# Optimization experiments

Hardware: AMD Instinct MI355X
Metric: run time of the kernel (lower is better)

## Reference

```python
import jax, jax.numpy as jnp
import numpy as np

ALPHA = 0.2  # LeakyReLU negative slope

B, K, F = 64, 100, 128   # batch, window_size (=num_nodes), n_features
E = 2 * K                 # embed_dim*2 = 200 (embed_dim defaults to window_size)


def setup_inputs() -> dict:
    key = jax.random.key(0)
    k1, k2, k3, k4, k5 = jax.random.split(key, 5)
    x = jax.random.normal(k1, (B, K, F), dtype=jnp.float32)
    # lin: Linear(2F -> E); store weight as (2F, E) so projection is x @ W
    W = jax.random.normal(k2, (2 * F, E), dtype=jnp.float32) * (1.0 / np.sqrt(2 * F))
    b = jax.random.normal(k3, (E,), dtype=jnp.float32) * 0.01
    # attention vector a: (E, 1) in torch; use (E,)
    a = jax.random.normal(k4, (E,), dtype=jnp.float32) * (1.414 / np.sqrt(E))
    bias = jax.random.normal(k5, (K, K), dtype=jnp.float32) * 0.01
    return {"x": x, "W": W, "b": b, "a": a, "bias": bias}


def reference(x, W, b, a, bias):
    F_ = x.shape[-1]
    # lin(concat(left, right)) == left @ W[:F] + right @ W[F:] + b;
    # compute the two projections once each instead of materializing the
    # (B, K, K, 2F) pairwise concat tensor.
    left_p = jnp.einsum('bkf,fe->bke', x, W[:F_])    # (B, K, E)
    right_p = jnp.einsum('bkf,fe->bke', x, W[F_:])   # (B, K, E)
    pre = left_p[:, :, None, :] + right_p[:, None, :, :] + b  # (B, K, K, E)
    act = jnp.where(pre > 0, pre, ALPHA * pre)                # LeakyReLU
    e = jnp.einsum('bije,e->bij', act, a) + bias              # (B, K, K)
    attention = jax.nn.softmax(e, axis=2)
    h = jax.nn.sigmoid(jnp.einsum('bij,bjf->bif', attention, x))  # (B, K, F)
    return h
```

## Files before the change

kernel.cpp:

```cpp
#include <hip/hip_runtime.h>

typedef _Float16 half_t;
typedef _Float16 h2 __attribute__((ext_vector_type(2)));
typedef unsigned int uint32;

#define K_ 100
#define F_ 128
#define E_ 200

#if defined(__has_builtin)
#if __has_builtin(__builtin_amdgcn_fdot2)
#define FDOT2(a,b,c) __builtin_amdgcn_fdot2((a),(b),(c),false)
#endif
#endif
#ifndef FDOT2
#define FDOT2(a,b,c) fmaf((float)(a).y,(float)(b).y, fmaf((float)(a).x,(float)(b).x,(c)))
#endif

__device__ __forceinline__ h2 bch2(uint32 u){ return __builtin_bit_cast(h2,u); }
__device__ __forceinline__ uint32 pkh2(float a, float b){
  h2 p; p.x=(half_t)a; p.y=(half_t)b; return __builtin_bit_cast(uint32,p);
}

#define LH_OFF 0
#define RH_OFF 640000
#define AH_OFF 1280000
#define AL_OFF 1280128
#define AR_OFF 1286528
#define XJ_OFF 1292928

__global__ __launch_bounds__(256) void k_proj(
    const float* __restrict__ x, const float* __restrict__ W,
    const float* __restrict__ bvec, const float* __restrict__ avec,
    uint32* __restrict__ ws)
{
  const int t  = threadIdx.x;
  const int r0 = (int)blockIdx.x * 10;

  __shared__ __align__(16) uint32 xsh[10 * 64];
  __shared__ float red[20][100];

  for (int u = t; u < 640; u += 256) {
    int row = u >> 6, f2 = u & 63;
    const float* xp = x + (size_t)(r0 + row) * F_ + 2 * f2;
    xsh[row * 64 + f2] = pkh2(xp[0], xp[1]);
  }
  if (blockIdx.x == 0 && t < 100)
    ws[AH_OFF + t] = pkh2(avec[2*t], avec[2*t+1]);
  __syncthreads();

  for (int u = t; u < 640; u += 256) {
    int f = u & 127, lp = u >> 7;
    uint32 u0 = xsh[(2*lp)     * 64 + (f >> 1)];
    uint32 u1 = xsh[(2*lp + 1) * 64 + (f >> 1)];
    int sh = (f & 1) * 16;
    ws[XJ_OFF + (size_t)(r0/2 + lp) * 128 + f] =
        ((u0 >> sh) & 0xffffu) | (((u1 >> sh) & 0xffffu) << 16);
  }

  if (t < 200) {
    const bool isR = (t >= 100);
    const int e2 = isR ? (t - 100) : t;
    const float* Wp = W + (size_t)(isR ? 128 : 0) * E_ + 2 * e2;

    float acc0[10], acc1[10];
    #pragma unroll
    for (int r = 0; r < 10; ++r) { acc0[r] = 0.f; acc1[r] = 0.f; }

    #pragma unroll
    for (int q = 0; q < 16; ++q) {
      uint32 w0u[4], w1u[4];
      #pragma unroll
      for (int fp = 0; fp < 4; ++fp) {
        const float* p0 = Wp + (size_t)(8*q + 2*fp) * E_;
        float2 Av = *(const float2*)p0;
        float2 Bv = *(const float2*)(p0 + E_);
        w0u[fp] = pkh2(Av.x, Bv.x);
        w1u[fp] = pkh2(Av.y, Bv.y);
      }
      #pragma unroll
      for (int r = 0; r < 10; ++r) {
        uint4 xq = *(const uint4*)(xsh + r * 64 + 4 * q);
        acc0[r] = FDOT2(bch2(xq.x), bch2(w0u[0]), acc0[r]);
        acc0[r] = FDOT2(bch2(xq.y), bch2(w0u[1]), acc0[r]);
        acc0[r] = FDOT2(bch2(xq.z), bch2(w0u[2]), acc0[r]);
        acc0[r] = FDOT2(bch2(xq.w), bch2(w0u[3]), acc0[r]);
        acc1[r] = FDOT2(bch2(xq.x), bch2(w1u[0]), acc1[r]);
        acc1[r] = FDOT2(bch2(xq.y), bch2(w1u[1]), acc1[r]);
        acc1[r] = FDOT2(bch2(xq.z), bch2(w1u[2]), acc1[r]);
        acc1[r] = FDOT2(bch2(xq.w), bch2(w1u[3]), acc1[r]);
      }
    }
    if (isR) {
      float b0 = bvec[2 * e2], b1 = bvec[2 * e2 + 1];
      #pragma unroll
      for (int r = 0; r < 10; ++r) { acc0[r] += b0; acc1[r] += b1; }
    }
    h2 a2 = bch2(pkh2(avec[2*e2], avec[2*e2+1]));
    uint32* dst = ws + (isR ? RH_OFF : LH_OFF);
    #pragma unroll
    for (int r = 0; r < 10; ++r) {
      uint32 pr = pkh2(acc0[r], acc1[r]);
      dst[(size_t)(r0 + r) * 100 + e2] = pr;
      red[(isR ? 10 : 0) + r][e2] = FDOT2(a2, bch2(pr), 0.f);
    }
  }
  __syncthreads();

  if (t < 20) {
    float s = 0.f;
    const float* rp = red[t];
    for (int k = 0; k < 100; ++k) s += rp[k];
    float* dstf = (float*)(ws + (t >= 10 ? AR_OFF : AL_OFF));
    dstf[r0 + (t % 10)] = s;
  }
}

#define STEP(lu, au, r0u, r1u, r2u, r3u)                                   \
  do {                                                                     \
    h2 a2 = bch2(au); h2 l2 = bch2(lu); h2 mm;                             \
    mm = __builtin_elementwise_min(l2 + bch2(r0u), z2); acc[0] = FDOT2(a2, mm, acc[0]); \
    mm = __builtin_elementwise_min(l2 + bch2(r1u), z2); acc[1] = FDOT2(a2, mm, acc[1]); \
    mm = __builtin_elementwise_min(l2 + bch2(r2u), z2); acc[2] = FDOT2(a2, mm, acc[2]); \
    mm = __builtin_elementwise_min(l2 + bch2(r3u), z2); acc[3] = FDOT2(a2, mm, acc[3]); \
  } while (0)

#define RPAD 104
#define LPAD 108

__global__ __launch_bounds__(256) void k_main(
    const float* __restrict__ x, const float* __restrict__ bias,
    const uint32* __restrict__ ws, float* __restrict__ out)
{
  const int t  = threadIdx.x;
  const int i0 = (int)blockIdx.x * 10;
  const int b  = (int)blockIdx.y;

  __shared__ __align__(16) uint32 Rsh[100 * RPAD];
  __shared__ __align__(16) uint32 Lsh[10 * LPAD];
  __shared__ uint32 Ash[100];
  __shared__ float  att[10 * 100];
  __shared__ uint32 att2[10 * 50];
  __shared__ float  scratch[256];
  __shared__ float  rowmax[10], rowinv[10];

  const bool act = (t < 250);
  const int ti = act ? (t % 10) : 0;
  const int tj = act ? (t / 10) : 0;

  {
    const uint32* Rb = ws + RH_OFF + (size_t)b * K_ * 100;
    for (int u = t; u < 2500; u += 256) {
      int row = u / 25, c4 = (u % 25) * 4;
      *(uint4*)(&Rsh[row * RPAD + c4]) = *(const uint4*)(Rb + (size_t)row * 100 + c4);
    }
    const uint32* Lb = ws + LH_OFF + (size_t)(b * K_ + i0) * 100;
    if (t < 250) {
      int row = t / 25, c4 = (t % 25) * 4;
      *(uint4*)(&Lsh[row * LPAD + c4]) = *(const uint4*)(Lb + (size_t)row * 100 + c4);
    }
    if (t < 100) Ash[t] = ws[AH_OFF + t];
  }
  __syncthreads();

  float acc[4] = {0.f,0.f,0.f,0.f};
  h2 z2; z2.x = (half_t)0; z2.y = (half_t)0;

  if (act) {
    const uint32* Lp  = Lsh + ti * LPAD;
    const uint32* Rp0 = Rsh + tj * RPAD;
    const uint32* Rp1 = Rsh + (tj + 25) * RPAD;
    const uint32* Rp2 = Rsh + (tj + 50) * RPAD;
    const uint32* Rp3 = Rsh + (tj + 75) * RPAD;
    #pragma unroll 5
    for (int q = 0; q < 25; ++q) {
      uint4 Lq  = *(const uint4*)(Lp  + 4*q);
      uint4 Aq  = *(const uint4*)(Ash + 4*q);
      uint4 R0q = *(const uint4*)(Rp0 + 4*q);
      uint4 R1q = *(const uint4*)(Rp1 + 4*q);
      uint4 R2q = *(const uint4*)(Rp2 + 4*q);
      uint4 R3q = *(const uint4*)(Rp3 + 4*q);
      STEP(Lq.x, Aq.x, R0q.x, R1q.x, R2q.x, R3q.x);
      STEP(Lq.y, Aq.y, R0q.y, R1q.y, R2q.y, R3q.y);
      STEP(Lq.z, Aq.z, R0q.z, R1q.z, R2q.z, R3q.z);
      STEP(Lq.w, Aq.w, R0q.w, R1q.w, R2q.w, R3q.w);
    }
  }

  float v[4];
  if (act) {
    const float* ALf = (const float*)(ws + AL_OFF);
    const float* ARf = (const float*)(ws + AR_OFF);
    float al = ALf[b*K_ + i0 + ti];
    #pragma unroll
    for (int s = 0; s < 4; ++s) {
      int j = tj + 25*s;
      float lv = al + ARf[b*K_ + j] + bias[(i0 + ti)*K_ + j] - 0.8f*acc[s];
      v[s] = fminf(fmaxf(lv, -30000.f), 30000.f);
    }
  }

  {
    float m = -3.0e38f;
    if (act) {
      #pragma unroll
      for (int s = 0; s < 4; ++s) m = fmaxf(m, v[s]);
    }
    scratch[t] = m;
    __syncthreads();
    if (t < 10) {
      float mm = scratch[t];
      for (int k = 1; k < 25; ++k) mm = fmaxf(mm, scratch[t + 10*k]);
      rowmax[t] = mm;
    }
    __syncthreads();
    float ssum = 0.f;
    if (act) {
      float m2 = rowmax[ti];
      #pragma unroll
      for (int s = 0; s < 4; ++s) ssum += __expf(v[s] - m2);
    }
    scratch[t] = ssum;
    __syncthreads();
    if (t < 10) {
      float s2 = 0.f;
      for (int k = 0; k < 25; ++k) s2 += scratch[t + 10*k];
      rowinv[t] = 1.f / s2;
    }
    __syncthreads();
  }
  if (act) {
    float m = rowmax[ti], inv = rowinv[ti];
    #pragma unroll
    for (int s = 0; s < 4; ++s)
      att[ti*K_ + tj + 25*s] = __expf(v[s] - m) * inv;
  }
  __syncthreads();
  for (int u = t; u < 500; u += 256) {
    int i = u / 50, jp = u - i*50;
    att2[i*50 + jp] = pkh2(att[i*K_ + 2*jp], att[i*K_ + 2*jp + 1]);
  }
  __syncthreads();

  {
    const int f = t & 127, ig = t >> 7;
    const uint32* XJ = ws + XJ_OFF + (size_t)(b*50) * 128;
    float z[5];
    #pragma unroll
    for (int m = 0; m < 5; ++m) z[m] = 0.f;
    for (int jp = 0; jp < 50; ++jp) {
      h2 xv = bch2(XJ[jp*128 + f]);
      #pragma unroll
      for (int m = 0; m < 5; ++m) {
        h2 av = bch2(att2[(ig*5 + m)*50 + jp]);
        z[m] = FDOT2(av, xv, z[m]);
      }
    }
    #pragma unroll
    for (int m = 0; m < 5; ++m) {
      int i = ig*5 + m;
      out[(size_t)(b*K_ + i0 + i)*F_ + f] = 1.f / (1.f + __expf(-z[m]));
    }
  }
}

extern "C" void kernel_launch(void* const* d_in, const int* in_sizes, int n_in,
                              void* d_out, int out_size, void* d_ws, size_t ws_size,
                              hipStream_t stream)
{
  const float* x    = (const float*)d_in[0];
  const float* W    = (const float*)d_in[1];
  const float* bvec = (const float*)d_in[2];
  const float* avec = (const float*)d_in[3];
  const float* bias = (const float*)d_in[4];
  float* out  = (float*)d_out;
  uint32* ws  = (uint32*)d_ws;

  k_proj<<<dim3(640),    dim3(256), 0, stream>>>(x, W, bvec, avec, ws);
  k_main<<<dim3(10, 64), dim3(256), 0, stream>>>(x, bias, ws, out);
}
```

Measured before the change: 98.35 us.

## Process two query rows per thread in k_main and parallelize projection reduction

Each k_main block now handles 20 query rows instead of 10, with every thread accumulating scores for two rows. This reuses each loaded R tile from shared memory across two rows and halves the number of times the per-batch R matrix is staged, while halving the grid to 320 blocks. The aggregation stage computes 10 output rows per thread. The 100-element serial sum at the end of k_proj is split into a two-level tree reduction. The cost is more registers and fewer blocks, which may reduce occupancy and load balance across CUs.

```diff
diff --git a/kernel.cpp b/kernel.cpp
--- a/kernel.cpp
+++ b/kernel.cpp
@@ -39,6 +39,7 @@
 
   __shared__ __align__(16) uint32 xsh[10 * 64];
   __shared__ float red[20][100];
+  __shared__ float red2[20 * 10];
 
   for (int u = t; u < 640; u += 256) {
     int row = u >> 6, f2 = u & 63;
@@ -107,22 +108,28 @@
   }
   __syncthreads();
 
+  if (t < 200) {
+    int rr = t / 10, seg = t % 10;
+    const float* rp = red[rr] + seg * 10;
+    float s = 0.f;
+    #pragma unroll
+    for (int k = 0; k < 10; ++k) s += rp[k];
+    red2[rr * 10 + seg] = s;
+  }
+  __syncthreads();
   if (t < 20) {
     float s = 0.f;
-    const float* rp = red[t];
-    for (int k = 0; k < 100; ++k) s += rp[k];
+    #pragma unroll
+    for (int k = 0; k < 10; ++k) s += red2[t * 10 + k];
     float* dstf = (float*)(ws + (t >= 10 ? AR_OFF : AL_OFF));
     dstf[r0 + (t % 10)] = s;
   }
 }
 
-#define STEP(lu, au, r0u, r1u, r2u, r3u)                                   \
+#define STEPA(A_, lu, au, ru)                                              \
   do {                                                                     \
-    h2 a2 = bch2(au); h2 l2 = bch2(lu); h2 mm;                             \
-    mm = __builtin_elementwise_min(l2 + bch2(r0u), z2); acc[0] = FDOT2(a2, mm, acc[0]); \
-    mm = __builtin_elementwise_min(l2 + bch2(r1u), z2); acc[1] = FDOT2(a2, mm, acc[1]); \
-    mm = __builtin_elementwise_min(l2 + bch2(r2u), z2); acc[2] = FDOT2(a2, mm, acc[2]); \
-    mm = __builtin_elementwise_min(l2 + bch2(r3u), z2); acc[3] = FDOT2(a2, mm, acc[3]); \
+    h2 mm = __builtin_elementwise_min(bch2(lu) + bch2(ru), z2);            \
+    A_ = FDOT2(bch2(au), mm, A_);                                          \
   } while (0)
 
 #define RPAD 104
@@ -133,19 +140,19 @@
     const uint32* __restrict__ ws, float* __restrict__ out)
 {
   const int t  = threadIdx.x;
-  const int i0 = (int)blockIdx.x * 10;
+  const int i0 = (int)blockIdx.x * 20;
   const int b  = (int)blockIdx.y;
 
   __shared__ __align__(16) uint32 Rsh[100 * RPAD];
-  __shared__ __align__(16) uint32 Lsh[10 * LPAD];
+  __shared__ __align__(16) uint32 Lsh[20 * LPAD];
   __shared__ uint32 Ash[100];
-  __shared__ float  att[10 * 100];
-  __shared__ uint32 att2[10 * 50];
-  __shared__ float  scratch[256];
-  __shared__ float  rowmax[10], rowinv[10];
+  __shared__ float  att[20 * 100];
+  __shared__ uint32 att2[20 * 50];
+  __shared__ float  scratch[512];
+  __shared__ float  rowmax[20], rowinv[20];
 
   const bool act = (t < 250);
-  const int ti = act ? (t % 10) : 0;
+  const int iq = act ? (t % 10) : 0;
   const int tj = act ? (t / 10) : 0;
 
   {
@@ -155,88 +162,118 @@
       *(uint4*)(&Rsh[row * RPAD + c4]) = *(const uint4*)(Rb + (size_t)row * 100 + c4);
     }
     const uint32* Lb = ws + LH_OFF + (size_t)(b * K_ + i0) * 100;
-    if (t < 250) {
-      int row = t / 25, c4 = (t % 25) * 4;
+    for (int u = t; u < 500; u += 256) {
+      int row = u / 25, c4 = (u % 25) * 4;
       *(uint4*)(&Lsh[row * LPAD + c4]) = *(const uint4*)(Lb + (size_t)row * 100 + c4);
     }
     if (t < 100) Ash[t] = ws[AH_OFF + t];
   }
   __syncthreads();
 
-  float acc[4] = {0.f,0.f,0.f,0.f};
+  float acc[2][4];
+  #pragma unroll
+  for (int p = 0; p < 2; ++p)
+    #pragma unroll
+    for (int s = 0; s < 4; ++s) acc[p][s] = 0.f;
   h2 z2; z2.x = (half_t)0; z2.y = (half_t)0;
 
   if (act) {
-    const uint32* Lp  = Lsh + ti * LPAD;
+    const uint32* Lp0 = Lsh + (2*iq)     * LPAD;
+    const uint32* Lp1 = Lsh + (2*iq + 1) * LPAD;
     const uint32* Rp0 = Rsh + tj * RPAD;
     const uint32* Rp1 = Rsh + (tj + 25) * RPAD;
     const uint32* Rp2 = Rsh + (tj + 50) * RPAD;
     const uint32* Rp3 = Rsh + (tj + 75) * RPAD;
     #pragma unroll 5
     for (int q = 0; q < 25; ++q) {
-      uint4 Lq  = *(const uint4*)(Lp  + 4*q);
+      uint4 L0q = *(const uint4*)(Lp0 + 4*q);
+      uint4 L1q = *(const uint4*)(Lp1 + 4*q);
       uint4 Aq  = *(const uint4*)(Ash + 4*q);
       uint4 R0q = *(const uint4*)(Rp0 + 4*q);
       uint4 R1q = *(const uint4*)(Rp1 + 4*q);
       uint4 R2q = *(const uint4*)(Rp2 + 4*q);
       uint4 R3q = *(const uint4*)(Rp3 + 4*q);
-      STEP(Lq.x, Aq.x, R0q.x, R1q.x, R2q.x, R3q.x);
-      STEP(Lq.y, Aq.y, R0q.y, R1q.y, R2q.y, R3q.y);
-      STEP(Lq.z, Aq.z, R0q.z, R1q.z, R2q.z, R3q.z);
-      STEP(Lq.w, Aq.w, R0q.w, R1q.w, R2q.w, R3q.w);
-    }
-  }
-
-  float v[4];
+      STEPA(acc[0][0], L0q.x, Aq.x, R0q.x); STEPA(acc[0][1], L0q.x, Aq.x, R1q.x);
+      STEPA(acc[0][2], L0q.x, Aq.x, R2q.x); STEPA(acc[0][3], L0q.x, Aq.x, R3q.x);
+      STEPA(acc[1][0], L1q.x, Aq.x, R0q.x); STEPA(acc[1][1], L1q.x, Aq.x, R1q.x);
+      STEPA(acc[1][2], L1q.x, Aq.x, R2q.x); STEPA(acc[1][3], L1q.x, Aq.x, R3q.x);
+      STEPA(acc[0][0], L0q.y, Aq.y, R0q.y); STEPA(acc[0][1], L0q.y, Aq.y, R1q.y);
+      STEPA(acc[0][2], L0q.y, Aq.y, R2q.y); STEPA(acc[0][3], L0q.y, Aq.y, R3q.y);
+      STEPA(acc[1][0], L1q.y, Aq.y, R0q.y); STEPA(acc[1][1], L1q.y, Aq.y, R1q.y);
+      STEPA(acc[1][2], L1q.y, Aq.y, R2q.y); STEPA(acc[1][3], L1q.y, Aq.y, R3q.y);
+      STEPA(acc[0][0], L0q.z, Aq.z, R0q.z); STEPA(acc[0][1], L0q.z, Aq.z, R1q.z);
+      STEPA(acc[0][2], L0q.z, Aq.z, R2q.z); STEPA(acc[0][3], L0q.z, Aq.z, R3q.z);
+      STEPA(acc[1][0], L1q.z, Aq.z, R0q.z); STEPA(acc[1][1], L1q.z, Aq.z, R1q.z);
+      STEPA(acc[1][2], L1q.z, Aq.z, R2q.z); STEPA(acc[1][3], L1q.z, Aq.z, R3q.z);
+      STEPA(acc[0][0], L0q.w, Aq.w, R0q.w); STEPA(acc[0][1], L0q.w, Aq.w, R1q.w);
+      STEPA(acc[0][2], L0q.w, Aq.w, R2q.w); STEPA(acc[0][3], L0q.w, Aq.w, R3q.w);
+      STEPA(acc[1][0], L1q.w, Aq.w, R0q.w); STEPA(acc[1][1], L1q.w, Aq.w, R1q.w);
+      STEPA(acc[1][2], L1q.w, Aq.w, R2q.w); STEPA(acc[1][3], L1q.w, Aq.w, R3q.w);
+    }
+  }
+
+  float v[2][4];
   if (act) {
     const float* ALf = (const float*)(ws + AL_OFF);
     const float* ARf = (const float*)(ws + AR_OFF);
-    float al = ALf[b*K_ + i0 + ti];
+    float al0 = ALf[b*K_ + i0 + 2*iq];
+    float al1 = ALf[b*K_ + i0 + 2*iq + 1];
     #pragma unroll
     for (int s = 0; s < 4; ++s) {
       int j = tj + 25*s;
-      float lv = al + ARf[b*K_ + j] + bias[(i0 + ti)*K_ + j] - 0.8f*acc[s];
-      v[s] = fminf(fmaxf(lv, -30000.f), 30000.f);
+      float arj = ARf[b*K_ + j];
+      float lv0 = al0 + arj + bias[(i0 + 2*iq)*K_ + j]     - 0.8f*acc[0][s];
+      float lv1 = al1 + arj + bias[(i0 + 2*iq + 1)*K_ + j] - 0.8f*acc[1][s];
+      v[0][s] = fminf(fmaxf(lv0, -30000.f), 30000.f);
+      v[1][s] = fminf(fmaxf(lv1, -30000.f), 30000.f);
     }
   }
 
   {
-    float m = -3.0e38f;
+    float m0 = -3.0e38f, m1 = -3.0e38f;
     if (act) {
       #pragma unroll
-      for (int s = 0; s < 4; ++s) m = fmaxf(m, v[s]);
-    }
-    scratch[t] = m;
+      for (int s = 0; s < 4; ++s) { m0 = fmaxf(m0, v[0][s]); m1 = fmaxf(m1, v[1][s]); }
+    }
+    scratch[t] = m0; scratch[256 + t] = m1;
     __syncthreads();
-    if (t < 10) {
-      float mm = scratch[t];
-      for (int k = 1; k < 25; ++k) mm = fmaxf(mm, scratch[t + 10*k]);
+    if (t < 20) {
+      int p = t & 1, iqr = t >> 1;
+      const float* sp = scratch + p*256 + iqr;
+      float mm = sp[0];
+      for (int k = 1; k < 25; ++k) mm = fmaxf(mm, sp[10*k]);
       rowmax[t] = mm;
     }
     __syncthreads();
-    float ssum = 0.f;
+    float e0 = 0.f, e1 = 0.f;
     if (act) {
-      float m2 = rowmax[ti];
-      #pragma unroll
-      for (int s = 0; s < 4; ++s) ssum += __expf(v[s] - m2);
-    }
-    scratch[t] = ssum;
+      float ma = rowmax[2*iq], mb = rowmax[2*iq + 1];
+      #pragma unroll
+      for (int s = 0; s < 4; ++s) { e0 += __expf(v[0][s] - ma); e1 += __expf(v[1][s] - mb); }
+    }
+    scratch[t] = e0; scratch[256 + t] = e1;
     __syncthreads();
-    if (t < 10) {
+    if (t < 20) {
+      int p = t & 1, iqr = t >> 1;
+      const float* sp = scratch + p*256 + iqr;
       float s2 = 0.f;
-      for (int k = 0; k < 25; ++k) s2 += scratch[t + 10*k];
+      for (int k = 0; k < 25; ++k) s2 += sp[10*k];
       rowinv[t] = 1.f / s2;
     }
     __syncthreads();
   }
   if (act) {
-    float m = rowmax[ti], inv = rowinv[ti];
-    #pragma unroll
-    for (int s = 0; s < 4; ++s)
-      att[ti*K_ + tj + 25*s] = __expf(v[s] - m) * inv;
-  }
-  __syncthreads();
-  for (int u = t; u < 500; u += 256) {
+    #pragma unroll
+    for (int p = 0; p < 2; ++p) {
+      int row = 2*iq + p;
+      float m = rowmax[row], inv = rowinv[row];
+      #pragma unroll
+      for (int s = 0; s < 4; ++s)
+        att[row*K_ + tj + 25*s] = __expf(v[p][s] - m) * inv;
+    }
+  }
+  __syncthreads();
+  for (int u = t; u < 1000; u += 256) {
     int i = u / 50, jp = u - i*50;
     att2[i*50 + jp] = pkh2(att[i*K_ + 2*jp], att[i*K_ + 2*jp + 1]);
   }
@@ -245,20 +282,20 @@
   {
     const int f = t & 127, ig = t >> 7;
     const uint32* XJ = ws + XJ_OFF + (size_t)(b*50) * 128;
-    float z[5];
-    #pragma unroll
-    for (int m = 0; m < 5; ++m) z[m] = 0.f;
+    float z[10];
+    #pragma unroll
+    for (int m = 0; m < 10; ++m) z[m] = 0.f;
     for (int jp = 0; jp < 50; ++jp) {
       h2 xv = bch2(XJ[jp*128 + f]);
       #pragma unroll
-      for (int m = 0; m < 5; ++m) {
-        h2 av = bch2(att2[(ig*5 + m)*50 + jp]);
+      for (int m = 0; m < 10; ++m) {
+        h2 av = bch2(att2[(ig*10 + m)*50 + jp]);
         z[m] = FDOT2(av, xv, z[m]);
       }
     }
     #pragma unroll
-    for (int m = 0; m < 5; ++m) {
-      int i = ig*5 + m;
+    for (int m = 0; m < 10; ++m) {
+      int i = ig*10 + m;
       out[(size_t)(b*K_ + i0 + i)*F_ + f] = 1.f / (1.f + __expf(-z[m]));
     }
   }
@@ -276,6 +313,6 @@
   float* out  = (float*)d_out;
   uint32* ws  = (uint32*)d_ws;
 
-  k_proj<<<dim3(640),    dim3(256), 0, stream>>>(x, W, bvec, avec, ws);
-  k_main<<<dim3(10, 64), dim3(256), 0, stream>>>(x, bias, ws, out);
+  k_proj<<<dim3(640),   dim3(256), 0, stream>>>(x, W, bvec, avec, ws);
+  k_main<<<dim3(5, 64), dim3(256), 0, stream>>>(x, bias, ws, out);
 }
```

Result: slower. 103.8 us (+5.5%).
